# Performance work log

Measured on AMD Instinct MI355X. Metric: run time of the kernel, lower is better.

## Reference

```python
import jax, jax.numpy as jnp
import numpy as np


def setup_inputs() -> dict:
    key = jax.random.key(0)
    k1, k2 = jax.random.split(key)
    B, C, H, L = 4, 1, 1024, 4096
    x = jax.random.normal(k1, (B, H, L), dtype=jnp.float32)
    k = jax.random.normal(k2, (C, H, L), dtype=jnp.float32)
    return {"x": x, "k": k}


def reference(x, k):
    # x: (B, H, L) input; k: (C, H, l_kernel) SSM convolution kernel.
    # FFT convolution with zero-padding to n = l_kernel + L (linear conv),
    # then truncate to the first L outputs (causal conv output).
    L = x.shape[-1]
    l_kernel = k.shape[-1]
    n = l_kernel + L
    k_f = jnp.fft.rfft(k, n=n)                       # (C, H, n//2+1) complex
    x_f = jnp.fft.rfft(x, n=n)                       # (B, H, n//2+1) complex
    y_f = jnp.einsum('bhl,chl->bchl', x_f, k_f)      # broadcast complex multiply
    y = jnp.fft.irfft(y_f, n=n)[..., :L]             # (B, C, H, L)
    return y
```

## Files before the change

kernel.cpp:

```cpp
#include <hip/hip_runtime.h>

#define THREADS 256
#define B_DIM   4
#define H_DIM   1024
#define L_DIM   4096
#define NFFT    4096
#define PI_F     3.14159265358979323846f
#define TWO_PI_F 6.28318530717958647692f

__device__ __forceinline__ float2 cmulf(float2 a, float2 b) {
    return make_float2(a.x*b.x - a.y*b.y, a.x*b.y + a.y*b.x);
}
__device__ __forceinline__ float2 caddf(float2 a, float2 b){ return make_float2(a.x+b.x, a.y+b.y); }
__device__ __forceinline__ float2 csubf(float2 a, float2 b){ return make_float2(a.x-b.x, a.y-b.y); }

__device__ __forceinline__ int swz(int i) { return i ^ ((i>>4)&15) ^ ((i>>8)&15); }

__device__ __forceinline__ float2 w16c(int q, float s) {
    constexpr float C[8] = {1.f, 0.9238795325f, 0.7071067812f, 0.3826834324f,
                            0.f, -0.3826834324f, -0.7071067812f, -0.9238795325f};
    constexpr float S[8] = {0.f, 0.3826834324f, 0.7071067812f, 0.9238795325f,
                            1.f, 0.9238795325f, 0.7071067812f, 0.3826834324f};
    return make_float2(C[q], s*S[q]);
}

template<int SGN>
__device__ __forceinline__ float2 twq(float2 d, int q) {
    if (q == 0) return d;
    if (q == 4) return make_float2((float)(-SGN)*d.y, (float)SGN*d.x);
    return cmulf(d, w16c(q, (float)SGN));
}

template<int SGN, bool HZ>
__device__ __forceinline__ void dif16(float2 v[16]) {
    if (HZ) {
        #pragma unroll
        for (int i = 0; i < 8; ++i) {
            float2 a = v[i];
            v[i+8] = twq<SGN>(a, i);
        }
    } else {
        #pragma unroll
        for (int i = 0; i < 8; ++i) {
            float2 a = v[i], b = v[i+8];
            v[i]   = caddf(a,b);
            v[i+8] = twq<SGN>(csubf(a,b), i);
        }
    }
    #pragma unroll
    for (int h = 4; h >= 1; h >>= 1) {
        const int step = 8 / h;
        #pragma unroll
        for (int g = 0; g < 16; g += 2*h) {
            #pragma unroll
            for (int i = 0; i < h; ++i) {
                float2 a = v[g+i], b = v[g+i+h];
                v[g+i]   = caddf(a,b);
                v[g+i+h] = twq<SGN>(csubf(a,b), i*step);
            }
        }
    }
}

template<int SGN>
__device__ __forceinline__ void dit16(float2 v[16]) {
    #pragma unroll
    for (int h = 1; h <= 8; h <<= 1) {
        const int step = 8 / h;
        #pragma unroll
        for (int g = 0; g < 16; g += 2*h) {
            #pragma unroll
            for (int i = 0; i < h; ++i) {
                float2 a = v[g+i];
                float2 b = twq<SGN>(v[g+i+h], i*step);
                v[g+i]   = caddf(a,b);
                v[g+i+h] = csubf(a,b);
            }
        }
    }
}

__global__ __launch_bounds__(THREADS, 2)
void fftconv_kernel(const float* __restrict__ x, const float* __restrict__ k,
                    float* __restrict__ out) {
    __shared__ float2 Zx[NFFT];
    __shared__ float2 Zk[NFFT];
    constexpr int REV4[16] = {0,8,4,12,2,10,6,14,1,9,5,13,3,11,7,15};

    const int t  = threadIdx.x;
    const int wg = blockIdx.x;
    const int hh = wg & (H_DIM - 1);
    const int b  = wg >> 10;

    const float2* xp = (const float2*)(x + ((size_t)(b*H_DIM + hh)) * L_DIM);
    const float2* kp = (const float2*)(k + (size_t)hh * L_DIM);

    float2 vx[16], vk[16];

    #pragma unroll
    for (int r = 0; r < 8; ++r) {
        vx[r] = xp[256*r + t];
        vk[r] = kp[256*r + t];
    }
    dif16<-1, true>(vx);
    dif16<-1, true>(vk);
    {
        const float base = -TWO_PI_F * (float)t / (float)NFFT;
        #pragma unroll
        for (int kk = 1; kk < 16; ++kk) {
            float sn, cs; __sincosf(base * (float)kk, &sn, &cs);
            float2 w = make_float2(cs, sn);
            vx[REV4[kk]] = cmulf(vx[REV4[kk]], w);
            vk[REV4[kk]] = cmulf(vk[REV4[kk]], w);
        }
    }
    #pragma unroll
    for (int kk = 0; kk < 16; ++kk) {
        int p = swz(256*kk + t);
        Zx[p] = vx[REV4[kk]];
        Zk[p] = vk[REV4[kk]];
    }
    __syncthreads();

    const int k1 = t >> 4, m = t & 15;
    const int rb = 256*k1 + m;
    #pragma unroll
    for (int r = 0; r < 16; ++r) {
        int p = swz(rb + 16*r);
        vx[r] = Zx[p]; vk[r] = Zk[p];
    }
    dif16<-1,false>(vx);
    dif16<-1,false>(vk);
    {
        const float base = -TWO_PI_F * (float)m / 256.f;
        #pragma unroll
        for (int kk = 1; kk < 16; ++kk) {
            float sn, cs; __sincosf(base * (float)kk, &sn, &cs);
            float2 w = make_float2(cs, sn);
            vx[REV4[kk]] = cmulf(vx[REV4[kk]], w);
            vk[REV4[kk]] = cmulf(vk[REV4[kk]], w);
        }
    }
    #pragma unroll
    for (int kk = 0; kk < 16; ++kk) {
        int p = swz(rb + 16*kk);
        Zx[p] = vx[REV4[kk]]; Zk[p] = vk[REV4[kk]];
    }
    __syncthreads();

    const int b3 = t << 4;
    #pragma unroll
    for (int r = 0; r < 16; ++r) {
        int p = swz(b3 + r);
        vx[r] = Zx[p]; vk[r] = Zk[p];
    }
    dif16<-1,false>(vx);
    dif16<-1,false>(vk);
    #pragma unroll
    for (int kk = 0; kk < 16; ++kk) {
        int p = swz(b3 + kk);
        Zx[p] = vx[REV4[kk]]; Zk[p] = vk[REV4[kk]];
    }
    __syncthreads();

    #pragma unroll
    for (int s = 0; s < 8; ++s) {
        int j = t + 256*s;
        if (j == 0) {
            float2 zx = Zx[0], zk = Zk[0];
            float ax0 = zx.x + zx.y, axM = zx.x - zx.y;
            float ak0 = zk.x + zk.y, akM = zk.x - zk.y;
            float y0 = ax0*ak0, yM = axM*akM;
            Zx[0] = make_float2(0.5f*(y0+yM), 0.5f*(y0-yM));
            int p2 = swz(8);
            float2 zx2 = Zx[p2], zk2 = Zk[p2];
            Zx[p2] = cmulf(zx2, zk2);
        } else {
            int jm = NFFT - j;
            int pj = swz( ((j&15)<<8)  | (((j>>4)&15)<<4)  | (j>>8)  );
            int pm = swz( ((jm&15)<<8) | (((jm>>4)&15)<<4) | (jm>>8) );
            float2 zxj = Zx[pj], zxm = Zx[pm];
            float2 zkj = Zk[pj], zkm = Zk[pm];

            float ang = -PI_F * (float)j / (float)NFFT;
            float sn, cs; __sincosf(ang, &sn, &cs);
            float2 w = make_float2(cs, sn);

            float2 Xe = make_float2(0.5f*(zxj.x + zxm.x), 0.5f*(zxj.y - zxm.y));
            float2 dx = make_float2(zxj.x - zxm.x, zxj.y + zxm.y);
            float2 Xo = make_float2(0.5f*dx.y, -0.5f*dx.x);
            float2 tx = cmulf(w, Xo);
            float2 Axj = caddf(Xe, tx);
            float2 Axm = make_float2(Xe.x - tx.x, -(Xe.y - tx.y));

            float2 Ke = make_float2(0.5f*(zkj.x + zkm.x), 0.5f*(zkj.y - zkm.y));
            float2 dk = make_float2(zkj.x - zkm.x, zkj.y + zkm.y);
            float2 Ko = make_float2(0.5f*dk.y, -0.5f*dk.x);
            float2 tk = cmulf(w, Ko);
            float2 Akj = caddf(Ke, tk);
            float2 Akm = make_float2(Ke.x - tk.x, -(Ke.y - tk.y));

            float2 Yj = cmulf(Axj, Akj);
            float2 Ym = cmulf(Axm, Akm);

            float2 u  = make_float2(0.5f*(Yj.x + Ym.x), 0.5f*(Yj.y - Ym.y));
            float2 dd = make_float2(Yj.x - Ym.x, Yj.y + Ym.y);
            float2 wc = make_float2(w.x, -w.y);
            float2 vv = cmulf(wc, dd);
            vv.x *= 0.5f; vv.y *= 0.5f;
            Zx[pj] = make_float2(u.x - vv.y, u.y + vv.x);
            Zx[pm] = make_float2(u.x + vv.y, -(u.y - vv.x));
        }
    }
    __syncthreads();

    #pragma unroll
    for (int r = 0; r < 16; ++r) vx[REV4[r]] = Zx[swz(b3 + r)];
    dit16<1>(vx);
    #pragma unroll
    for (int mm = 0; mm < 16; ++mm) Zx[swz(b3 + mm)] = vx[mm];
    __syncthreads();

    {
        const float base = TWO_PI_F * (float)m / 256.f;
        #pragma unroll
        for (int kk = 0; kk < 16; ++kk) {
            float2 val = Zx[swz(rb + 16*kk)];
            if (kk > 0) {
                float sn, cs; __sincosf(base * (float)kk, &sn, &cs);
                val = cmulf(val, make_float2(cs, sn));
            }
            vx[REV4[kk]] = val;
        }
        dit16<1>(vx);
        #pragma unroll
        for (int r = 0; r < 16; ++r) Zx[swz(rb + 16*r)] = vx[r];
    }
    __syncthreads();

    {
        const float base = TWO_PI_F * (float)t / (float)NFFT;
        #pragma unroll
        for (int kk = 0; kk < 16; ++kk) {
            float2 val = Zx[swz(256*kk + t)];
            if (kk > 0) {
                float sn, cs; __sincosf(base * (float)kk, &sn, &cs);
                val = cmulf(val, make_float2(cs, sn));
            }
            vx[REV4[kk]] = val;
        }
        dit16<1>(vx);
        float2* op = (float2*)(out + ((size_t)(b*H_DIM + hh)) * L_DIM);
        const float sc = 1.f / (float)NFFT;
        #pragma unroll
        for (int n1 = 0; n1 < 8; ++n1) {
            float2 z = vx[n1];
            op[256*n1 + t] = make_float2(z.x*sc, z.y*sc);
        }
    }
}

extern "C" void kernel_launch(void* const* d_in, const int* in_sizes, int n_in,
                              void* d_out, int out_size, void* d_ws, size_t ws_size,
                              hipStream_t stream) {
    const float* x = (const float*)d_in[0];
    const float* k = (const float*)d_in[1];
    float* out = (float*)d_out;
    fftconv_kernel<<<dim3(B_DIM * H_DIM), dim3(THREADS), 0, stream>>>(x, k, out);
}
```

Before: 193.4 us.

## Precompute kernel spectrum once per channel and generate twiddles by recurrence

Splits the work into a per-channel kernel FFT that writes the unpacked spectrum to workspace and a main kernel that runs only the x FFT, the pointwise multiply and the inverse FFT. The kernel FFT is no longer repeated for each of the 4 batches, and halving shared memory raises the occupancy target to 4 blocks. Twiddles are now built from one sincos plus complex-multiply powers instead of 15 sincos calls, which may cost a little accuracy. It adds a 32 MB spectrum write and read through global memory, and falls back to the old fused path if the workspace is too small.

```diff
diff --git a/kernel.cpp b/kernel.cpp
--- a/kernel.cpp
+++ b/kernel.cpp
@@ -15,6 +15,25 @@
 __device__ __forceinline__ float2 csubf(float2 a, float2 b){ return make_float2(a.x-b.x, a.y-b.y); }
 
 __device__ __forceinline__ int swz(int i) { return i ^ ((i>>4)&15) ^ ((i>>8)&15); }
+
+__device__ __forceinline__ void make_tw(float base, float2 w[16]) {
+    float sn, cs; __sincosf(base, &sn, &cs);
+    w[1]  = make_float2(cs, sn);
+    w[2]  = cmulf(w[1], w[1]);
+    w[3]  = cmulf(w[2], w[1]);
+    w[4]  = cmulf(w[2], w[2]);
+    w[5]  = cmulf(w[4], w[1]);
+    w[6]  = cmulf(w[4], w[2]);
+    w[7]  = cmulf(w[4], w[3]);
+    w[8]  = cmulf(w[4], w[4]);
+    w[9]  = cmulf(w[8], w[1]);
+    w[10] = cmulf(w[8], w[2]);
+    w[11] = cmulf(w[8], w[3]);
+    w[12] = cmulf(w[8], w[4]);
+    w[13] = cmulf(w[8], w[5]);
+    w[14] = cmulf(w[8], w[6]);
+    w[15] = cmulf(w[8], w[7]);
+}
 
 __device__ __forceinline__ float2 w16c(int q, float s) {
     constexpr float C[8] = {1.f, 0.9238795325f, 0.7071067812f, 0.3826834324f,
@@ -80,11 +99,83 @@
     }
 }
 
-__global__ __launch_bounds__(THREADS, 2)
-void fftconv_kernel(const float* __restrict__ x, const float* __restrict__ k,
-                    float* __restrict__ out) {
+__device__ __constant__ int REV4_C[16] = {0,8,4,12,2,10,6,14,1,9,5,13,3,11,7,15};
+
+__device__ __forceinline__ void fwd_fft_row(const float2* __restrict__ src, float2* Z, int t) {
+    constexpr int REV4[16] = {0,8,4,12,2,10,6,14,1,9,5,13,3,11,7,15};
+    float2 v[16], w[16];
+    #pragma unroll
+    for (int r = 0; r < 8; ++r) v[r] = src[256*r + t];
+    dif16<-1, true>(v);
+    make_tw(-TWO_PI_F * (float)t / (float)NFFT, w);
+    #pragma unroll
+    for (int kk = 1; kk < 16; ++kk) v[REV4[kk]] = cmulf(v[REV4[kk]], w[kk]);
+    #pragma unroll
+    for (int kk = 0; kk < 16; ++kk) Z[swz(256*kk + t)] = v[REV4[kk]];
+    __syncthreads();
+
+    const int k1 = t >> 4, m = t & 15;
+    const int rb = 256*k1 + m;
+    #pragma unroll
+    for (int r = 0; r < 16; ++r) v[r] = Z[swz(rb + 16*r)];
+    dif16<-1,false>(v);
+    make_tw(-TWO_PI_F * (float)m / 256.f, w);
+    #pragma unroll
+    for (int kk = 1; kk < 16; ++kk) v[REV4[kk]] = cmulf(v[REV4[kk]], w[kk]);
+    #pragma unroll
+    for (int kk = 0; kk < 16; ++kk) Z[swz(rb + 16*kk)] = v[REV4[kk]];
+    __syncthreads();
+
+    const int b3 = t << 4;
+    #pragma unroll
+    for (int r = 0; r < 16; ++r) v[r] = Z[swz(b3 + r)];
+    dif16<-1,false>(v);
+    #pragma unroll
+    for (int kk = 0; kk < 16; ++kk) Z[swz(b3 + kk)] = v[REV4[kk]];
+}
+
+__device__ __forceinline__ int binpos(int j) {
+    return swz( ((j&15)<<8) | (((j>>4)&15)<<4) | (j>>8) );
+}
+
+__global__ __launch_bounds__(THREADS, 4)
+void kfft_kernel(const float* __restrict__ k, float2* __restrict__ Kf_all) {
+    __shared__ float2 Zk[NFFT];
+    const int t  = threadIdx.x;
+    const int hh = blockIdx.x;
+    const float2* kp = (const float2*)(k + (size_t)hh * L_DIM);
+
+    fwd_fft_row(kp, Zk, t);
+    __syncthreads();
+
+    float2* Kf = Kf_all + (size_t)hh * NFFT;
+    #pragma unroll
+    for (int s = 0; s < 8; ++s) {
+        int j = t + 256*s;
+        if (j == 0) {
+            float2 zk = Zk[0];
+            Kf[0] = make_float2(zk.x + zk.y, zk.x - zk.y);
+            float2 zk2 = Zk[swz(8)];
+            Kf[2048] = make_float2(zk2.x, -zk2.y);
+        } else {
+            int jm = NFFT - j;
+            float2 zkj = Zk[binpos(j)], zkm = Zk[binpos(jm)];
+            float sn, cs; __sincosf(-PI_F * (float)j / (float)NFFT, &sn, &cs);
+            float2 w = make_float2(cs, sn);
+            float2 Ke = make_float2(0.5f*(zkj.x + zkm.x), 0.5f*(zkj.y - zkm.y));
+            float2 dk = make_float2(zkj.x - zkm.x, zkj.y + zkm.y);
+            float2 Ko = make_float2(0.5f*dk.y, -0.5f*dk.x);
+            float2 tk = cmulf(w, Ko);
+            Kf[j]  = caddf(Ke, tk);
+            Kf[jm] = make_float2(Ke.x - tk.x, -(Ke.y - tk.y));
+        }
+    }
+}
+
+__global__ __launch_bounds__(THREADS, 4)
+void conv_main_kernel(const float* __restrict__ x, const float2* __restrict__ Kf_all,
+                      float* __restrict__ out) {
     __shared__ float2 Zx[NFFT];
-    __shared__ float2 Zk[NFFT];
     constexpr int REV4[16] = {0,8,4,12,2,10,6,14,1,9,5,13,3,11,7,15};
 
     const int t  = threadIdx.x;
@@ -93,74 +184,119 @@
     const int b  = wg >> 10;
 
     const float2* xp = (const float2*)(x + ((size_t)(b*H_DIM + hh)) * L_DIM);
-    const float2* kp = (const float2*)(k + (size_t)hh * L_DIM);
-
-    float2 vx[16], vk[16];
-
-    #pragma unroll
-    for (int r = 0; r < 8; ++r) {
-        vx[r] = xp[256*r + t];
-        vk[r] = kp[256*r + t];
-    }
-    dif16<-1, true>(vx);
-    dif16<-1, true>(vk);
-    {
-        const float base = -TWO_PI_F * (float)t / (float)NFFT;
-        #pragma unroll
-        for (int kk = 1; kk < 16; ++kk) {
-            float sn, cs; __sincosf(base * (float)kk, &sn, &cs);
+    const float2* Kf = Kf_all + (size_t)hh * NFFT;
+
+    fwd_fft_row(xp, Zx, t);
+
+    float2 kfj[8], kfm[8], kf2;
+    #pragma unroll
+    for (int s = 0; s < 8; ++s) {
+        int j = t + 256*s;
+        kfj[s] = Kf[j];
+        kfm[s] = Kf[(NFFT - j) & (NFFT - 1)];
+    }
+    kf2 = Kf[2048];
+    __syncthreads();
+
+    #pragma unroll
+    for (int s = 0; s < 8; ++s) {
+        int j = t + 256*s;
+        if (j == 0) {
+            float2 zx = Zx[0];
+            float ax0 = zx.x + zx.y, axM = zx.x - zx.y;
+            float y0 = ax0 * kfj[0].x, yM = axM * kfj[0].y;
+            Zx[0] = make_float2(0.5f*(y0 + yM), 0.5f*(y0 - yM));
+            int p2 = swz(8);
+            float2 zx2 = Zx[p2];
+            Zx[p2] = cmulf(zx2, make_float2(kf2.x, -kf2.y));
+        } else {
+            int jm = NFFT - j;
+            int pj = binpos(j), pm = binpos(jm);
+            float2 zxj = Zx[pj], zxm = Zx[pm];
+
+            float sn, cs; __sincosf(-PI_F * (float)j / (float)NFFT, &sn, &cs);
             float2 w = make_float2(cs, sn);
-            vx[REV4[kk]] = cmulf(vx[REV4[kk]], w);
-            vk[REV4[kk]] = cmulf(vk[REV4[kk]], w);
-        }
-    }
-    #pragma unroll
-    for (int kk = 0; kk < 16; ++kk) {
-        int p = swz(256*kk + t);
-        Zx[p] = vx[REV4[kk]];
-        Zk[p] = vk[REV4[kk]];
-    }
-    __syncthreads();
-
+
+            float2 Xe = make_float2(0.5f*(zxj.x + zxm.x), 0.5f*(zxj.y - zxm.y));
+            float2 dx = make_float2(zxj.x - zxm.x, zxj.y + zxm.y);
+            float2 Xo = make_float2(0.5f*dx.y, -0.5f*dx.x);
+            float2 tx = cmulf(w, Xo);
+            float2 Axj = caddf(Xe, tx);
+            float2 Axm = make_float2(Xe.x - tx.x, -(Xe.y - tx.y));
+
+            float2 Yj = cmulf(Axj, kfj[s]);
+            float2 Ym = cmulf(Axm, kfm[s]);
+
+            float2 u  = make_float2(0.5f*(Yj.x + Ym.x), 0.5f*(Yj.y - Ym.y));
+            float2 dd = make_float2(Yj.x - Ym.x, Yj.y + Ym.y);
+            float2 wc = make_float2(w.x, -w.y);
+            float2 vv = cmulf(wc, dd);
+            vv.x *= 0.5f; vv.y *= 0.5f;
+            Zx[pj] = make_float2(u.x - vv.y, u.y + vv.x);
+            Zx[pm] = make_float2(u.x + vv.y, -(u.y - vv.x));
+        }
+    }
+    __syncthreads();
+
+    float2 vx[16], w[16];
     const int k1 = t >> 4, m = t & 15;
     const int rb = 256*k1 + m;
-    #pragma unroll
-    for (int r = 0; r < 16; ++r) {
-        int p = swz(rb + 16*r);
-        vx[r] = Zx[p]; vk[r] = Zk[p];
-    }
-    dif16<-1,false>(vx);
-    dif16<-1,false>(vk);
-    {
-        const float base = -TWO_PI_F * (float)m / 256.f;
-        #pragma unroll
-        for (int kk = 1; kk < 16; ++kk) {
-            float sn, cs; __sincosf(base * (float)kk, &sn, &cs);
-            float2 w = make_float2(cs, sn);
-            vx[REV4[kk]] = cmulf(vx[REV4[kk]], w);
-            vk[REV4[kk]] = cmulf(vk[REV4[kk]], w);
-        }
-    }
+    const int b3 = t << 4;
+
+    #pragma unroll
+    for (int r = 0; r < 16; ++r) vx[REV4[r]] = Zx[swz(b3 + r)];
+    dit16<1>(vx);
+    #pragma unroll
+    for (int mm = 0; mm < 16; ++mm) Zx[swz(b3 + mm)] = vx[mm];
+    __syncthreads();
+
+    make_tw(TWO_PI_F * (float)m / 256.f, w);
     #pragma unroll
     for (int kk = 0; kk < 16; ++kk) {
-        int p = swz(rb + 16*kk);
-        Zx[p] = vx[REV4[kk]]; Zk[p] = vk[REV4[kk]];
-    }
-    __syncthreads();
-
-    const int b3 = t << 4;
-    #pragma unroll
-    for (int r = 0; r < 16; ++r) {
-        int p = swz(b3 + r);
-        vx[r] = Zx[p]; vk[r] = Zk[p];
-    }
-    dif16<-1,false>(vx);
-    dif16<-1,false>(vk);
+        float2 val = Zx[swz(rb + 16*kk)];
+        if (kk > 0) val = cmulf(val, w[kk]);
+        vx[REV4[kk]] = val;
+    }
+    dit16<1>(vx);
+    #pragma unroll
+    for (int r = 0; r < 16; ++r) Zx[swz(rb + 16*r)] = vx[r];
+    __syncthreads();
+
+    make_tw(TWO_PI_F * (float)t / (float)NFFT, w);
     #pragma unroll
     for (int kk = 0; kk < 16; ++kk) {
-        int p = swz(b3 + kk);
-        Zx[p] = vx[REV4[kk]]; Zk[p] = vk[REV4[kk]];
-    }
+        float2 val = Zx[swz(256*kk + t)];
+        if (kk > 0) val = cmulf(val, w[kk]);
+        vx[REV4[kk]] = val;
+    }
+    dit16<1>(vx);
+    float2* op = (float2*)(out + ((size_t)(b*H_DIM + hh)) * L_DIM);
+    const float sc = 1.f / (float)NFFT;
+    #pragma unroll
+    for (int n1 = 0; n1 < 8; ++n1) {
+        float2 z = vx[n1];
+        op[256*n1 + t] = make_float2(z.x*sc, z.y*sc);
+    }
+}
+
+__global__ __launch_bounds__(THREADS, 2)
+void fftconv_fallback(const float* __restrict__ x, const float* __restrict__ k,
+                      float* __restrict__ out) {
+    __shared__ float2 Zx[NFFT];
+    __shared__ float2 Zk[NFFT];
+    constexpr int REV4[16] = {0,8,4,12,2,10,6,14,1,9,5,13,3,11,7,15};
+
+    const int t  = threadIdx.x;
+    const int wg = blockIdx.x;
+    const int hh = wg & (H_DIM - 1);
+    const int b  = wg >> 10;
+
+    const float2* xp = (const float2*)(x + ((size_t)(b*H_DIM + hh)) * L_DIM);
+    const float2* kp = (const float2*)(k + (size_t)hh * L_DIM);
+
+    fwd_fft_row(xp, Zx, t);
+    __syncthreads();
+    fwd_fft_row(kp, Zk, t);
     __syncthreads();
 
     #pragma unroll
@@ -173,36 +309,28 @@
             float y0 = ax0*ak0, yM = axM*akM;
             Zx[0] = make_float2(0.5f*(y0+yM), 0.5f*(y0-yM));
             int p2 = swz(8);
-            float2 zx2 = Zx[p2], zk2 = Zk[p2];
-            Zx[p2] = cmulf(zx2, zk2);
+            Zx[p2] = cmulf(Zx[p2], Zk[p2]);
         } else {
             int jm = NFFT - j;
-            int pj = swz( ((j&15)<<8)  | (((j>>4)&15)<<4)  | (j>>8)  );
-            int pm = swz( ((jm&15)<<8) | (((jm>>4)&15)<<4) | (jm>>8) );
+            int pj = binpos(j), pm = binpos(jm);
             float2 zxj = Zx[pj], zxm = Zx[pm];
             float2 zkj = Zk[pj], zkm = Zk[pm];
-
-            float ang = -PI_F * (float)j / (float)NFFT;
-            float sn, cs; __sincosf(ang, &sn, &cs);
+            float sn, cs; __sincosf(-PI_F * (float)j / (float)NFFT, &sn, &cs);
             float2 w = make_float2(cs, sn);
-
             float2 Xe = make_float2(0.5f*(zxj.x + zxm.x), 0.5f*(zxj.y - zxm.y));
             float2 dx = make_float2(zxj.x - zxm.x, zxj.y + zxm.y);
             float2 Xo = make_float2(0.5f*dx.y, -0.5f*dx.x);
             float2 tx = cmulf(w, Xo);
             float2 Axj = caddf(Xe, tx);
             float2 Axm = make_float2(Xe.x - tx.x, -(Xe.y - tx.y));
-
             float2 Ke = make_float2(0.5f*(zkj.x + zkm.x), 0.5f*(zkj.y - zkm.y));
             float2 dk = make_float2(zkj.x - zkm.x, zkj.y + zkm.y);
             float2 Ko = make_float2(0.5f*dk.y, -0.5f*dk.x);
             float2 tk = cmulf(w, Ko);
             float2 Akj = caddf(Ke, tk);
             float2 Akm = make_float2(Ke.x - tk.x, -(Ke.y - tk.y));
-
             float2 Yj = cmulf(Axj, Akj);
             float2 Ym = cmulf(Axm, Akm);
-
             float2 u  = make_float2(0.5f*(Yj.x + Ym.x), 0.5f*(Yj.y - Ym.y));
             float2 dd = make_float2(Yj.x - Ym.x, Yj.y + Ym.y);
             float2 wc = make_float2(w.x, -w.y);
@@ -214,6 +342,11 @@
     }
     __syncthreads();
 
+    float2 vx[16], w[16];
+    const int k1 = t >> 4, m = t & 15;
+    const int rb = 256*k1 + m;
+    const int b3 = t << 4;
+
     #pragma unroll
     for (int r = 0; r < 16; ++r) vx[REV4[r]] = Zx[swz(b3 + r)];
     dit16<1>(vx);
@@ -221,42 +354,32 @@
     for (int mm = 0; mm < 16; ++mm) Zx[swz(b3 + mm)] = vx[mm];
     __syncthreads();
 
-    {
-        const float base = TWO_PI_F * (float)m / 256.f;
-        #pragma unroll
-        for (int kk = 0; kk < 16; ++kk) {
-            float2 val = Zx[swz(rb + 16*kk)];
-            if (kk > 0) {
-                float sn, cs; __sincosf(base * (float)kk, &sn, &cs);
-                val = cmulf(val, make_float2(cs, sn));
-            }
-            vx[REV4[kk]] = val;
-        }
-        dit16<1>(vx);
-        #pragma unroll
-        for (int r = 0; r < 16; ++r) Zx[swz(rb + 16*r)] = vx[r];
-    }
-    __syncthreads();
-
-    {
-        const float base = TWO_PI_F * (float)t / (float)NFFT;
-        #pragma unroll
-        for (int kk = 0; kk < 16; ++kk) {
-            float2 val = Zx[swz(256*kk + t)];
-            if (kk > 0) {
-                float sn, cs; __sincosf(base * (float)kk, &sn, &cs);
-                val = cmulf(val, make_float2(cs, sn));
-            }
-            vx[REV4[kk]] = val;
-        }
-        dit16<1>(vx);
-        float2* op = (float2*)(out + ((size_t)(b*H_DIM + hh)) * L_DIM);
-        const float sc = 1.f / (float)NFFT;
-        #pragma unroll
-        for (int n1 = 0; n1 < 8; ++n1) {
-            float2 z = vx[n1];
-            op[256*n1 + t] = make_float2(z.x*sc, z.y*sc);
-        }
+    make_tw(TWO_PI_F * (float)m / 256.f, w);
+    #pragma unroll
+    for (int kk = 0; kk < 16; ++kk) {
+        float2 val = Zx[swz(rb + 16*kk)];
+        if (kk > 0) val = cmulf(val, w[kk]);
+        vx[REV4[kk]] = val;
+    }
+    dit16<1>(vx);
+    #pragma unroll
+    for (int r = 0; r < 16; ++r) Zx[swz(rb + 16*r)] = vx[r];
+    __syncthreads();
+
+    make_tw(TWO_PI_F * (float)t / (float)NFFT, w);
+    #pragma unroll
+    for (int kk = 0; kk < 16; ++kk) {
+        float2 val = Zx[swz(256*kk + t)];
+        if (kk > 0) val = cmulf(val, w[kk]);
+        vx[REV4[kk]] = val;
+    }
+    dit16<1>(vx);
+    float2* op = (float2*)(out + ((size_t)(b*H_DIM + hh)) * L_DIM);
+    const float sc = 1.f / (float)NFFT;
+    #pragma unroll
+    for (int n1 = 0; n1 < 8; ++n1) {
+        float2 z = vx[n1];
+        op[256*n1 + t] = make_float2(z.x*sc, z.y*sc);
     }
 }
 
@@ -266,5 +389,12 @@
     const float* x = (const float*)d_in[0];
     const float* k = (const float*)d_in[1];
     float* out = (float*)d_out;
-    fftconv_kernel<<<dim3(B_DIM * H_DIM), dim3(THREADS), 0, stream>>>(x, k, out);
-}
+    const size_t need = (size_t)H_DIM * NFFT * sizeof(float2);
+    if (ws_size >= need) {
+        float2* Kf = (float2*)d_ws;
+        kfft_kernel<<<dim3(H_DIM), dim3(THREADS), 0, stream>>>(k, Kf);
+        conv_main_kernel<<<dim3(B_DIM * H_DIM), dim3(THREADS), 0, stream>>>(x, Kf, out);
+    } else {
+        fftconv_fallback<<<dim3(B_DIM * H_DIM), dim3(THREADS), 0, stream>>>(x, k, out);
+    }
+}
```

After: 176.4 us. -8.8%, faster.
